# Optimization experiments

Measured on AMD Instinct MI355X. Metric: run time of the kernel, lower is better.

Reference implementation:

```python
import jax, jax.numpy as jnp
import numpy as np

HEAD_SIZE = 64

def setup_inputs() -> dict:
    key = jax.random.key(0)
    k1, k2, k3, k4 = jax.random.split(key, 4)
    B, S, D = 8, 2048, 1024
    scale = 1.0 / np.sqrt(D)
    x = jax.random.normal(k1, (B, S, D), dtype=jnp.float32)
    Wk = jax.random.normal(k2, (D, HEAD_SIZE), dtype=jnp.float32) * scale
    Wq = jax.random.normal(k3, (D, HEAD_SIZE), dtype=jnp.float32) * scale
    Wv = jax.random.normal(k4, (D, HEAD_SIZE), dtype=jnp.float32) * scale
    return {"x": x, "Wk": Wk, "Wq": Wq, "Wv": Wv}

def reference(x, Wk, Wq, Wv):
    # x: [B, S, D]; projections to [B, S, H]
    k = jnp.einsum('bsd,dh->bsh', x, Wk)
    q = jnp.einsum('bsd,dh->bsh', x, Wq)
    v = jnp.einsum('bsd,dh->bsh', x, Wv)
    H = q.shape[-1]
    scores = jnp.einsum('bqh,bkh->bqk', q, k) / jnp.sqrt(jnp.float32(H))  # [B,S,S]
    S = scores.shape[-1]
    causal = jnp.tril(jnp.ones((S, S), dtype=bool))
    scores = jnp.where(causal, scores, -jnp.inf)
    attn = jax.nn.softmax(scores, axis=-1)
    z = jnp.einsum('bqk,bkh->bqh', attn, v)  # [B,S,H]
    return z
```

## Files before the change

### kernel.cpp

```cpp
#include <hip/hip_runtime.h>
#include <hip/hip_bf16.h>

#define B_ 8
#define S_ 2048
#define D_ 1024
#define H_ 64

typedef __attribute__((ext_vector_type(8))) short bf16x8;
typedef __attribute__((ext_vector_type(4))) float f32x4;
typedef __attribute__((ext_vector_type(4))) unsigned short u16x4;
typedef unsigned short u16;
typedef unsigned int u32;

#define QSCALE 0.18033688011112042f

static __device__ __forceinline__ u16 f2bf(float f) {
  union { float f; unsigned u; } v; v.f = f;
  unsigned r = v.u + 0x7FFFu + ((v.u >> 16) & 1u);
  return (u16)(r >> 16);
}

__global__ __launch_bounds__(256) void wprep_kernel(const float* __restrict__ Wk,
                                                    const float* __restrict__ Wq,
                                                    const float* __restrict__ Wv,
                                                    u16* __restrict__ Wt) {
  __shared__ float lds[64][65];
  const int wsel = blockIdx.x >> 4;
  const int d0 = (blockIdx.x & 15) << 6;
  const float* W = (wsel == 0) ? Wq : ((wsel == 1) ? Wk : Wv);
  const int cbase = wsel << 6;
  const int tid = threadIdx.x;

#pragma unroll
  for (int e = 0; e < 16; ++e) {
    const int idx = e * 256 + tid;
    const int dd = idx >> 6, h = idx & 63;
    lds[dd][h] = W[(size_t)(d0 + dd) * H_ + h];
  }
  __syncthreads();
#pragma unroll
  for (int e = 0; e < 16; ++e) {
    const int idx = e * 256 + tid;
    const int c = idx >> 6, dd = idx & 63;
    Wt[(size_t)(cbase + c) * D_ + d0 + dd] = f2bf(lds[dd][c]);
  }
}

__global__ __launch_bounds__(512, 4) void qkv_kernel(const float* __restrict__ x,
                                                     const u16* __restrict__ Wt,
                                                     u16* __restrict__ Qb,
                                                     u16* __restrict__ Kb,
                                                     u16* __restrict__ Vt) {
  __shared__ char sh[65536];
  char* const xsb = sh;
  char* const wsb = sh + 16384;

  const int tid = threadIdx.x;
  const int w = tid >> 6;
  const int lane = tid & 63;
  const int r = lane & 15;
  const int g = lane >> 4;
  const int rg = w >> 2;
  const int cg = w & 3;

  const int bpin = blockIdx.x & 7;
  const int jj = blockIdx.x >> 3;
  const long row0 = ((long)bpin * 64 + jj) * 32;

#define STAGE_X(kc, buf)                                                       \
  {                                                                            \
    const char* gb = (const char*)x + (size_t)row0 * 4096 + (size_t)(kc) * 256;\
    const int L = tid * 16;                                                    \
    const int row = L >> 8;                                                    \
    const int sw = (L & 255) ^ ((row & 7) << 4);                               \
    __builtin_amdgcn_global_load_lds(                                          \
        (const __attribute__((address_space(1))) u32*)(gb + (size_t)row * 4096 + sw), \
        (__attribute__((address_space(3))) u32*)(xsb + (buf) * 8192 + L),      \
        16, 0, 0);                                                             \
  }

#define STAGE_W(kc, buf)                                                       \
  {                                                                            \
    const char* gb = (const char*)Wt + (size_t)(kc) * 128;                     \
    _Pragma("unroll") for (int j2 = 0; j2 < 3; ++j2) {                         \
      const int L = j2 * 8192 + tid * 16;                                      \
      const int col = L >> 7;                                                  \
      const int sw = (L & 127) ^ ((col & 7) << 4);                             \
      __builtin_amdgcn_global_load_lds(                                        \
          (const __attribute__((address_space(1))) u32*)(gb + (size_t)col * 2048 + sw), \
          (__attribute__((address_space(3))) u32*)(wsb + (buf) * 24576 + L),   \
          16, 0, 0);                                                           \
    }                                                                          \
  }

  f32x4 acc[3];
#pragma unroll
  for (int nf = 0; nf < 3; ++nf) acc[nf] = (f32x4){0.f, 0.f, 0.f, 0.f};

  STAGE_X(0, 0);
  STAGE_W(0, 0);
  int cur = 0;

  const int rr = rg * 16 + r;
  const int xswz = (rr & 7) << 4;

  for (int kc = 0; kc < 16; ++kc) {
    __syncthreads();
    if (kc < 15) {
      STAGE_X(kc + 1, cur ^ 1);
      STAGE_W(kc + 1, cur ^ 1);
    }
    __builtin_amdgcn_sched_barrier(0);

    const char* xb = xsb + cur * 8192;
    const char* wb = wsb + cur * 24576;
#pragma unroll
    for (int ks = 0; ks < 2; ++ks) {
      const int cb = ks * 128 + g * 32;
      const float4 lo = *(const float4*)(xb + rr * 256 + (cb ^ xswz));
      const float4 hi = *(const float4*)(xb + rr * 256 + ((cb + 16) ^ xswz));
      bf16x8 a;
      a[0] = (short)f2bf(lo.x); a[1] = (short)f2bf(lo.y);
      a[2] = (short)f2bf(lo.z); a[3] = (short)f2bf(lo.w);
      a[4] = (short)f2bf(hi.x); a[5] = (short)f2bf(hi.y);
      a[6] = (short)f2bf(hi.z); a[7] = (short)f2bf(hi.w);
#pragma unroll
      for (int nf = 0; nf < 3; ++nf) {
        const int col = cg * 48 + nf * 16 + r;
        const int wcb = (ks * 64 + g * 16) ^ ((col & 7) << 4);
        const bf16x8 b = *(const bf16x8*)(wb + col * 128 + wcb);
        acc[nf] = __builtin_amdgcn_mfma_f32_16x16x32_bf16(a, b, acc[nf], 0, 0, 0);
      }
    }
    cur ^= 1;
  }
#undef STAGE_W
#undef STAGE_X

  const int bb = (int)(row0 >> 11);
  const int srow = (int)(row0 & 2047) + rg * 16;
#pragma unroll
  for (int nf = 0; nf < 3; ++nf) {
    const int col = cg * 48 + nf * 16 + r;
    if (col < 64) {
#pragma unroll
      for (int ii = 0; ii < 4; ++ii)
        Qb[(row0 + rg * 16 + 4 * g + ii) * H_ + col] = f2bf(acc[nf][ii] * QSCALE);
    } else if (col < 128) {
#pragma unroll
      for (int ii = 0; ii < 4; ++ii)
        Kb[(row0 + rg * 16 + 4 * g + ii) * H_ + (col - 64)] = f2bf(acc[nf][ii]);
    } else {
      u16x4 vp;
#pragma unroll
      for (int ii = 0; ii < 4; ++ii) vp[ii] = f2bf(acc[nf][ii]);
      *(u16x4*)(Vt + ((size_t)(bb * H_ + (col - 128))) * S_ + srow + 4 * g) = vp;
    }
  }
}

__global__ __launch_bounds__(256, 2) void attn7_kernel(const u16* __restrict__ Qb,
                                                       const u16* __restrict__ Kb,
                                                       const u16* __restrict__ Vt,
                                                       float* __restrict__ out) {
  __shared__ u16 plds[4][16 * 72];
  __shared__ float plo[4][16][68];
  __shared__ float pml[4][2][16];

  const int b = blockIdx.x & 7;
  const int j = blockIdx.x >> 3;
  const int w = threadIdx.x >> 6;
  const int lane = threadIdx.x & 63;
  const int r = lane & 15;
  const int g = lane >> 4;

  const int qt = (w < 2) ? j : (127 - j);
  const int s = w & 1;
  const int q0 = qt << 4;
  const int T = (qt >> 2) + 1;
  const int half = (T + 1) >> 1;
  const int start = s ? half : 0;
  const int end = s ? T : half;

  const u16* Qp = Qb + ((long)(b * S_ + q0 + r)) * H_ + 8 * g;
  const bf16x8 bq0 = *(const bf16x8*)Qp;
  const bf16x8 bq1 = *(const bf16x8*)(Qp + 32);

  const u16* Kbase = Kb + (long)b * S_ * H_ + (long)r * H_ + 8 * g;
  const u16* Vbase = Vt + (long)b * H_ * S_ + (long)r * S_ + 8 * g;

  f32x4 o[4];
#pragma unroll
  for (int nf = 0; nf < 4; ++nf) o[nf] = (f32x4){0.f, 0.f, 0.f, 0.f};
  float m = -INFINITY, l = 0.f;

  u16* pw = plds[w];

  bf16x8 ka[8];
  if (start < end) {
    const int k0 = start << 6;
#pragma unroll
    for (int kf = 0; kf < 4; ++kf) {
      const u16* Kp = Kbase + (long)(k0 + kf * 16) * H_;
      ka[2 * kf] = *(const bf16x8*)(Kp);
      ka[2 * kf + 1] = *(const bf16x8*)(Kp + 32);
    }
  }

  for (int kt = start; kt < end; ++kt) {
    const int k0 = kt << 6;

    f32x4 t4[4];
    __builtin_amdgcn_s_setprio(1);
#pragma unroll
    for (int kf = 0; kf < 4; ++kf) {
      f32x4 t = (f32x4){0.f, 0.f, 0.f, 0.f};
      t = __builtin_amdgcn_mfma_f32_16x16x32_bf16(ka[2 * kf], bq0, t, 0, 0, 0);
      t = __builtin_amdgcn_mfma_f32_16x16x32_bf16(ka[2 * kf + 1], bq1, t, 0, 0, 0);
      t4[kf] = t;
    }
    __builtin_amdgcn_s_setprio(0);

    bf16x8 vv[8];
#pragma unroll
    for (int nf = 0; nf < 4; ++nf) {
      const u16* Vp = Vbase + (long)(nf * 16) * S_ + k0;
      vv[2 * nf] = *(const bf16x8*)(Vp);
      vv[2 * nf + 1] = *(const bf16x8*)(Vp + 32);
    }
    if (kt + 1 < end) {
      const int kn = (kt + 1) << 6;
#pragma unroll
      for (int kf = 0; kf < 4; ++kf) {
        const u16* Kp = Kbase + (long)(kn + kf * 16) * H_;
        ka[2 * kf] = *(const bf16x8*)(Kp);
        ka[2 * kf + 1] = *(const bf16x8*)(Kp + 32);
      }
    }

    if (kt == T - 1) {
#pragma unroll
      for (int kf = 0; kf < 4; ++kf)
#pragma unroll
        for (int i = 0; i < 4; ++i) {
          const int k = k0 + kf * 16 + 4 * g + i;
          if (k > q0 + r) t4[kf][i] = -INFINITY;
        }
    }

    float pm = t4[0][0];
#pragma unroll
    for (int kf = 0; kf < 4; ++kf)
#pragma unroll
      for (int i = 0; i < 4; ++i) pm = fmaxf(pm, t4[kf][i]);
    pm = fmaxf(pm, __shfl_xor(pm, 16));
    pm = fmaxf(pm, __shfl_xor(pm, 32));

    if (__any(pm > m + 8.f)) {
      const float mn = fmaxf(m, pm);
      const float sc = exp2f(m - mn);
      m = mn;
      l *= sc;
      float scr[4];
#pragma unroll
      for (int i = 0; i < 4; ++i) scr[i] = __shfl(sc, 4 * g + i);
#pragma unroll
      for (int nf = 0; nf < 4; ++nf)
#pragma unroll
        for (int i = 0; i < 4; ++i) o[nf][i] *= scr[i];
    }

    float ps = 0.f;
#pragma unroll
    for (int kf = 0; kf < 4; ++kf)
#pragma unroll
      for (int i = 0; i < 4; ++i) {
        const float p = exp2f(t4[kf][i] - m);
        t4[kf][i] = p;
        ps += p;
      }
    ps += __shfl_xor(ps, 16);
    ps += __shfl_xor(ps, 32);
    l += ps;

#pragma unroll
    for (int kf = 0; kf < 4; ++kf) {
      u16x4 pk;
#pragma unroll
      for (int i = 0; i < 4; ++i) pk[i] = f2bf(t4[kf][i]);
      *(u16x4*)(pw + r * 72 + kf * 16 + 4 * g) = pk;
    }

    const bf16x8 pa0 = *(const bf16x8*)(pw + r * 72 + 8 * g);
    const bf16x8 pa1 = *(const bf16x8*)(pw + r * 72 + 32 + 8 * g);

    __builtin_amdgcn_s_setprio(1);
#pragma unroll
    for (int nf = 0; nf < 4; ++nf) {
      o[nf] = __builtin_amdgcn_mfma_f32_16x16x32_bf16(pa0, vv[2 * nf], o[nf], 0, 0, 0);
      o[nf] = __builtin_amdgcn_mfma_f32_16x16x32_bf16(pa1, vv[2 * nf + 1], o[nf], 0, 0, 0);
    }
    __builtin_amdgcn_s_setprio(0);
  }

#pragma unroll
  for (int nf = 0; nf < 4; ++nf)
#pragma unroll
    for (int i = 0; i < 4; ++i)
      plo[w][4 * g + i][nf * 16 + r] = o[nf][i];
  if (g == 0) {
    pml[w][0][r] = m;
    pml[w][1][r] = l;
  }
  __syncthreads();

  const int base = (w >> 1) << 1;
  const int hlf = w & 1;
  const int qq0 = ((base == 0) ? j : (127 - j)) << 4;
#pragma unroll
  for (int rr = 0; rr < 8; ++rr) {
    const int row = hlf * 8 + rr;
    const float mA = pml[base][0][row], mB = pml[base + 1][0][row];
    const float lA = pml[base][1][row], lB = pml[base + 1][1][row];
    const float M = fmaxf(mA, mB);
    const float ea = exp2f(mA - M), eb = exp2f(mB - M);
    const float inv = 1.f / (lA * ea + lB * eb);
    const float oo = plo[base][row][lane] * ea + plo[base + 1][row][lane] * eb;
    out[((long)(b * S_ + qq0 + row)) * H_ + lane] = oo * inv;
  }
}

extern "C" void kernel_launch(void* const* d_in, const int* in_sizes, int n_in,
                              void* d_out, int out_size, void* d_ws, size_t ws_size,
                              hipStream_t stream) {
  const float* x  = (const float*)d_in[0];
  const float* Wk = (const float*)d_in[1];
  const float* Wq = (const float*)d_in[2];
  const float* Wv = (const float*)d_in[3];
  float* out = (float*)d_out;

  u16* Qb = (u16*)d_ws;
  u16* Kb = Qb + (long)B_ * S_ * H_;
  u16* Vt = Kb + (long)B_ * S_ * H_;
  u16* Wt = Vt + (long)B_ * S_ * H_;

  wprep_kernel<<<48, 256, 0, stream>>>(Wk, Wq, Wv, Wt);
  qkv_kernel<<<512, 512, 0, stream>>>(x, Wt, Qb, Kb, Vt);
  attn7_kernel<<<B_ * 64, 256, 0, stream>>>(Qb, Kb, Vt, out);
}
```

Measured before the change: 60.42 us.

## Pre-swizzle weights into MFMA fragment layout and load directly to registers in QKV projection

Measured after the change: 67.75 us. +12.1%, slower.

```diff
diff --git a/kernel.cpp b/kernel.cpp
--- a/kernel.cpp
+++ b/kernel.cpp
@@ -23,7 +23,7 @@
 __global__ __launch_bounds__(256) void wprep_kernel(const float* __restrict__ Wk,
                                                     const float* __restrict__ Wq,
                                                     const float* __restrict__ Wv,
-                                                    u16* __restrict__ Wt) {
+                                                    u16* __restrict__ Wt2) {
   __shared__ float lds[64][65];
   const int wsel = blockIdx.x >> 4;
   const int d0 = (blockIdx.x & 15) << 6;
@@ -34,122 +34,129 @@
 #pragma unroll
   for (int e = 0; e < 16; ++e) {
     const int idx = e * 256 + tid;
-    const int dd = idx >> 6, h = idx & 63;
-    lds[dd][h] = W[(size_t)(d0 + dd) * H_ + h];
+    lds[idx >> 6][idx & 63] = W[(size_t)(d0 + (idx >> 6)) * H_ + (idx & 63)];
   }
   __syncthreads();
-#pragma unroll
-  for (int e = 0; e < 16; ++e) {
-    const int idx = e * 256 + tid;
-    const int c = idx >> 6, dd = idx & 63;
-    Wt[(size_t)(cbase + c) * D_ + d0 + dd] = f2bf(lds[dd][c]);
-  }
-}
-
-__global__ __launch_bounds__(512, 4) void qkv_kernel(const float* __restrict__ x,
-                                                     const u16* __restrict__ Wt,
+
+#pragma unroll
+  for (int t2 = 0; t2 < 2; ++t2) {
+    const int idx = t2 * 256 + tid;
+    const int c_local = idx >> 3;
+    const int o = idx & 7;
+    const int c = cbase + c_local;
+    const int wv = c / 48, rem = c % 48;
+    const int nf = rem >> 4, rr = rem & 15;
+    const int k0 = d0 + o * 8;
+    const int step = k0 >> 5;
+    const int gg = (k0 >> 3) & 3;
+    u16 vals[8];
+#pragma unroll
+    for (int j = 0; j < 8; ++j) vals[j] = f2bf(lds[o * 8 + j][c_local]);
+    u16* dst = Wt2 + ((size_t)((step * 4 + wv) * 3 + nf) * 64 + gg * 16 + rr) * 8;
+    u16x4 v0 = {vals[0], vals[1], vals[2], vals[3]};
+    u16x4 v1 = {vals[4], vals[5], vals[6], vals[7]};
+    *(u16x4*)dst = v0;
+    *(u16x4*)(dst + 4) = v1;
+  }
+}
+
+__global__ __launch_bounds__(256, 2) void qkv_kernel(const float* __restrict__ x,
+                                                     const u16* __restrict__ Wt2,
                                                      u16* __restrict__ Qb,
                                                      u16* __restrict__ Kb,
                                                      u16* __restrict__ Vt) {
-  __shared__ char sh[65536];
-  char* const xsb = sh;
-  char* const wsb = sh + 16384;
+  __shared__ char xlds[65536];
 
   const int tid = threadIdx.x;
   const int w = tid >> 6;
   const int lane = tid & 63;
   const int r = lane & 15;
   const int g = lane >> 4;
-  const int rg = w >> 2;
-  const int cg = w & 3;
 
   const int bpin = blockIdx.x & 7;
   const int jj = blockIdx.x >> 3;
-  const long row0 = ((long)bpin * 64 + jj) * 32;
-
-#define STAGE_X(kc, buf)                                                       \
-  {                                                                            \
-    const char* gb = (const char*)x + (size_t)row0 * 4096 + (size_t)(kc) * 256;\
-    const int L = tid * 16;                                                    \
-    const int row = L >> 8;                                                    \
-    const int sw = (L & 255) ^ ((row & 7) << 4);                               \
-    __builtin_amdgcn_global_load_lds(                                          \
-        (const __attribute__((address_space(1))) u32*)(gb + (size_t)row * 4096 + sw), \
-        (__attribute__((address_space(3))) u32*)(xsb + (buf) * 8192 + L),      \
-        16, 0, 0);                                                             \
-  }
-
-#define STAGE_W(kc, buf)                                                       \
-  {                                                                            \
-    const char* gb = (const char*)Wt + (size_t)(kc) * 128;                     \
-    _Pragma("unroll") for (int j2 = 0; j2 < 3; ++j2) {                         \
-      const int L = j2 * 8192 + tid * 16;                                      \
-      const int col = L >> 7;                                                  \
-      const int sw = (L & 127) ^ ((col & 7) << 4);                             \
-      __builtin_amdgcn_global_load_lds(                                        \
-          (const __attribute__((address_space(1))) u32*)(gb + (size_t)col * 2048 + sw), \
-          (__attribute__((address_space(3))) u32*)(wsb + (buf) * 24576 + L),   \
-          16, 0, 0);                                                           \
-    }                                                                          \
+  const long row0 = ((long)bpin * 128 + jj) * 16;
+
+  {
+    const char* gb = (const char*)x + (size_t)row0 * 4096;
+#pragma unroll
+    for (int j = 0; j < 16; ++j) {
+      const int off = (tid * 16) ^ ((j & 7) << 4);
+      __builtin_amdgcn_global_load_lds(
+          (const __attribute__((address_space(1))) u32*)(gb + (size_t)j * 4096 + off),
+          (__attribute__((address_space(3))) u32*)(xlds + j * 4096 + tid * 16),
+          16, 0, 0);
+    }
   }
 
   f32x4 acc[3];
-#pragma unroll
-  for (int nf = 0; nf < 3; ++nf) acc[nf] = (f32x4){0.f, 0.f, 0.f, 0.f};
-
-  STAGE_X(0, 0);
-  STAGE_W(0, 0);
-  int cur = 0;
-
-  const int rr = rg * 16 + r;
-  const int xswz = (rr & 7) << 4;
-
-  for (int kc = 0; kc < 16; ++kc) {
-    __syncthreads();
-    if (kc < 15) {
-      STAGE_X(kc + 1, cur ^ 1);
-      STAGE_W(kc + 1, cur ^ 1);
-    }
-    __builtin_amdgcn_sched_barrier(0);
-
-    const char* xb = xsb + cur * 8192;
-    const char* wb = wsb + cur * 24576;
-#pragma unroll
-    for (int ks = 0; ks < 2; ++ks) {
-      const int cb = ks * 128 + g * 32;
-      const float4 lo = *(const float4*)(xb + rr * 256 + (cb ^ xswz));
-      const float4 hi = *(const float4*)(xb + rr * 256 + ((cb + 16) ^ xswz));
+  acc[0] = acc[1] = acc[2] = (f32x4){0.f, 0.f, 0.f, 0.f};
+
+  const u16* wp = Wt2 + (size_t)(w * 3) * 512 + lane * 8;
+  bf16x8 wA[3], wB[3];
+#pragma unroll
+  for (int nf = 0; nf < 3; ++nf) wA[nf] = *(const bf16x8*)(wp + nf * 512);
+#pragma unroll
+  for (int nf = 0; nf < 3; ++nf) wB[nf] = *(const bf16x8*)(wp + 6144 + nf * 512);
+
+  __syncthreads();
+
+  const int xswz = (r & 7) << 4;
+  const char* xrow = xlds + r * 4096;
+
+#pragma unroll
+  for (int s2 = 0; s2 < 16; ++s2) {
+    {
+      const int off = (2 * s2) * 128 + g * 32;
+      const float4 lo = *(const float4*)(xrow + (off ^ xswz));
+      const float4 hi = *(const float4*)(xrow + ((off + 16) ^ xswz));
       bf16x8 a;
       a[0] = (short)f2bf(lo.x); a[1] = (short)f2bf(lo.y);
       a[2] = (short)f2bf(lo.z); a[3] = (short)f2bf(lo.w);
       a[4] = (short)f2bf(hi.x); a[5] = (short)f2bf(hi.y);
       a[6] = (short)f2bf(hi.z); a[7] = (short)f2bf(hi.w);
 #pragma unroll
-      for (int nf = 0; nf < 3; ++nf) {
-        const int col = cg * 48 + nf * 16 + r;
-        const int wcb = (ks * 64 + g * 16) ^ ((col & 7) << 4);
-        const bf16x8 b = *(const bf16x8*)(wb + col * 128 + wcb);
-        acc[nf] = __builtin_amdgcn_mfma_f32_16x16x32_bf16(a, b, acc[nf], 0, 0, 0);
-      }
-    }
-    cur ^= 1;
-  }
-#undef STAGE_W
-#undef STAGE_X
-
-  const int bb = (int)(row0 >> 11);
-  const int srow = (int)(row0 & 2047) + rg * 16;
+      for (int nf = 0; nf < 3; ++nf)
+        acc[nf] = __builtin_amdgcn_mfma_f32_16x16x32_bf16(a, wA[nf], acc[nf], 0, 0, 0);
+    }
+    if (s2 < 15) {
+#pragma unroll
+      for (int nf = 0; nf < 3; ++nf)
+        wA[nf] = *(const bf16x8*)(wp + (size_t)(2 * s2 + 2) * 6144 + nf * 512);
+    }
+    {
+      const int off = (2 * s2 + 1) * 128 + g * 32;
+      const float4 lo = *(const float4*)(xrow + (off ^ xswz));
+      const float4 hi = *(const float4*)(xrow + ((off + 16) ^ xswz));
+      bf16x8 a;
+      a[0] = (short)f2bf(lo.x); a[1] = (short)f2bf(lo.y);
+      a[2] = (short)f2bf(lo.z); a[3] = (short)f2bf(lo.w);
+      a[4] = (short)f2bf(hi.x); a[5] = (short)f2bf(hi.y);
+      a[6] = (short)f2bf(hi.z); a[7] = (short)f2bf(hi.w);
+#pragma unroll
+      for (int nf = 0; nf < 3; ++nf)
+        acc[nf] = __builtin_amdgcn_mfma_f32_16x16x32_bf16(a, wB[nf], acc[nf], 0, 0, 0);
+    }
+    if (s2 < 15) {
+#pragma unroll
+      for (int nf = 0; nf < 3; ++nf)
+        wB[nf] = *(const bf16x8*)(wp + (size_t)(2 * s2 + 3) * 6144 + nf * 512);
+    }
+  }
+
+  const int bb = bpin;
+  const int srow = (int)(row0 & 2047);
 #pragma unroll
   for (int nf = 0; nf < 3; ++nf) {
-    const int col = cg * 48 + nf * 16 + r;
+    const int col = w * 48 + nf * 16 + r;
     if (col < 64) {
 #pragma unroll
       for (int ii = 0; ii < 4; ++ii)
-        Qb[(row0 + rg * 16 + 4 * g + ii) * H_ + col] = f2bf(acc[nf][ii] * QSCALE);
+        Qb[(row0 + 4 * g + ii) * H_ + col] = f2bf(acc[nf][ii] * QSCALE);
     } else if (col < 128) {
 #pragma unroll
       for (int ii = 0; ii < 4; ++ii)
-        Kb[(row0 + rg * 16 + 4 * g + ii) * H_ + (col - 64)] = f2bf(acc[nf][ii]);
+        Kb[(row0 + 4 * g + ii) * H_ + (col - 64)] = f2bf(acc[nf][ii]);
     } else {
       u16x4 vp;
 #pragma unroll
@@ -342,9 +349,9 @@
   u16* Qb = (u16*)d_ws;
   u16* Kb = Qb + (long)B_ * S_ * H_;
   u16* Vt = Kb + (long)B_ * S_ * H_;
-  u16* Wt = Vt + (long)B_ * S_ * H_;
-
-  wprep_kernel<<<48, 256, 0, stream>>>(Wk, Wq, Wv, Wt);
-  qkv_kernel<<<512, 512, 0, stream>>>(x, Wt, Qb, Kb, Vt);
+  u16* Wt2 = Vt + (long)B_ * S_ * H_;
+
+  wprep_kernel<<<48, 256, 0, stream>>>(Wk, Wq, Wv, Wt2);
+  qkv_kernel<<<1024, 256, 0, stream>>>(x, Wt2, Qb, Kb, Vt);
   attn7_kernel<<<B_ * 64, 256, 0, stream>>>(Qb, Kb, Vt, out);
 }
```

## Balance causal attention work evenly across four waves per block

Applied to the files above, without the earlier changes.

After: 61.03 us. About the same (+1.0%).

```diff
diff --git a/kernel.cpp b/kernel.cpp
--- a/kernel.cpp
+++ b/kernel.cpp
@@ -137,7 +137,7 @@
 #undef STAGE_W
 #undef STAGE_X
 
-  const int bb = (int)(row0 >> 11);
+  const int bb = bpin;
   const int srow = (int)(row0 & 2047) + rg * 16;
 #pragma unroll
   for (int nf = 0; nf < 3; ++nf) {
@@ -159,13 +159,13 @@
   }
 }
 
-__global__ __launch_bounds__(256, 2) void attn7_kernel(const u16* __restrict__ Qb,
+__global__ __launch_bounds__(256, 2) void attn9_kernel(const u16* __restrict__ Qb,
                                                        const u16* __restrict__ Kb,
                                                        const u16* __restrict__ Vt,
                                                        float* __restrict__ out) {
   __shared__ u16 plds[4][16 * 72];
-  __shared__ float plo[4][16][68];
-  __shared__ float pml[4][2][16];
+  __shared__ float plo[8][16][68];
+  __shared__ float pml[8][2][16];
 
   const int b = blockIdx.x & 7;
   const int j = blockIdx.x >> 3;
@@ -174,158 +174,165 @@
   const int r = lane & 15;
   const int g = lane >> 4;
 
-  const int qt = (w < 2) ? j : (127 - j);
-  const int s = w & 1;
-  const int q0 = qt << 4;
-  const int T = (qt >> 2) + 1;
-  const int half = (T + 1) >> 1;
-  const int start = s ? half : 0;
-  const int end = s ? T : half;
-
-  const u16* Qp = Qb + ((long)(b * S_ + q0 + r)) * H_ + 8 * g;
-  const bf16x8 bq0 = *(const bf16x8*)Qp;
-  const bf16x8 bq1 = *(const bf16x8*)(Qp + 32);
+  const int qtA = j, qtB = 127 - j;
+  const int T_A = (qtA >> 2) + 1;
+  const int T_B = (qtB >> 2) + 1;
+  const int start = (w * 33) >> 2;
+  const int end = ((w + 1) * 33) >> 2;
+
+  const u16* QpA = Qb + ((long)(b * S_ + (qtA << 4) + r)) * H_ + 8 * g;
+  const bf16x8 bqA0 = *(const bf16x8*)QpA;
+  const bf16x8 bqA1 = *(const bf16x8*)(QpA + 32);
+  const u16* QpB = Qb + ((long)(b * S_ + (qtB << 4) + r)) * H_ + 8 * g;
+  const bf16x8 bqB0 = *(const bf16x8*)QpB;
+  const bf16x8 bqB1 = *(const bf16x8*)(QpB + 32);
 
   const u16* Kbase = Kb + (long)b * S_ * H_ + (long)r * H_ + 8 * g;
   const u16* Vbase = Vt + (long)b * H_ * S_ + (long)r * S_ + 8 * g;
 
-  f32x4 o[4];
-#pragma unroll
-  for (int nf = 0; nf < 4; ++nf) o[nf] = (f32x4){0.f, 0.f, 0.f, 0.f};
-  float m = -INFINITY, l = 0.f;
-
   u16* pw = plds[w];
 
-  bf16x8 ka[8];
-  if (start < end) {
-    const int k0 = start << 6;
-#pragma unroll
-    for (int kf = 0; kf < 4; ++kf) {
-      const u16* Kp = Kbase + (long)(k0 + kf * 16) * H_;
-      ka[2 * kf] = *(const bf16x8*)(Kp);
-      ka[2 * kf + 1] = *(const bf16x8*)(Kp + 32);
-    }
-  }
-
-  for (int kt = start; kt < end; ++kt) {
-    const int k0 = kt << 6;
-
-    f32x4 t4[4];
-    __builtin_amdgcn_s_setprio(1);
-#pragma unroll
-    for (int kf = 0; kf < 4; ++kf) {
-      f32x4 t = (f32x4){0.f, 0.f, 0.f, 0.f};
-      t = __builtin_amdgcn_mfma_f32_16x16x32_bf16(ka[2 * kf], bq0, t, 0, 0, 0);
-      t = __builtin_amdgcn_mfma_f32_16x16x32_bf16(ka[2 * kf + 1], bq1, t, 0, 0, 0);
-      t4[kf] = t;
-    }
-    __builtin_amdgcn_s_setprio(0);
-
-    bf16x8 vv[8];
-#pragma unroll
-    for (int nf = 0; nf < 4; ++nf) {
-      const u16* Vp = Vbase + (long)(nf * 16) * S_ + k0;
-      vv[2 * nf] = *(const bf16x8*)(Vp);
-      vv[2 * nf + 1] = *(const bf16x8*)(Vp + 32);
-    }
-    if (kt + 1 < end) {
-      const int kn = (kt + 1) << 6;
-#pragma unroll
-      for (int kf = 0; kf < 4; ++kf) {
-        const u16* Kp = Kbase + (long)(kn + kf * 16) * H_;
-        ka[2 * kf] = *(const bf16x8*)(Kp);
-        ka[2 * kf + 1] = *(const bf16x8*)(Kp + 32);
-      }
-    }
-
-    if (kt == T - 1) {
-#pragma unroll
-      for (int kf = 0; kf < 4; ++kf)
-#pragma unroll
-        for (int i = 0; i < 4; ++i) {
-          const int k = k0 + kf * 16 + 4 * g + i;
-          if (k > q0 + r) t4[kf][i] = -INFINITY;
-        }
-    }
-
-    float pm = t4[0][0];
-#pragma unroll
-    for (int kf = 0; kf < 4; ++kf)
-#pragma unroll
-      for (int i = 0; i < 4; ++i) pm = fmaxf(pm, t4[kf][i]);
-    pm = fmaxf(pm, __shfl_xor(pm, 16));
-    pm = fmaxf(pm, __shfl_xor(pm, 32));
-
-    if (__any(pm > m + 8.f)) {
-      const float mn = fmaxf(m, pm);
-      const float sc = exp2f(m - mn);
-      m = mn;
-      l *= sc;
-      float scr[4];
-#pragma unroll
-      for (int i = 0; i < 4; ++i) scr[i] = __shfl(sc, 4 * g + i);
-#pragma unroll
-      for (int nf = 0; nf < 4; ++nf)
-#pragma unroll
-        for (int i = 0; i < 4; ++i) o[nf][i] *= scr[i];
-    }
-
-    float ps = 0.f;
-#pragma unroll
-    for (int kf = 0; kf < 4; ++kf)
-#pragma unroll
-      for (int i = 0; i < 4; ++i) {
-        const float p = exp2f(t4[kf][i] - m);
-        t4[kf][i] = p;
-        ps += p;
-      }
-    ps += __shfl_xor(ps, 16);
-    ps += __shfl_xor(ps, 32);
-    l += ps;
-
-#pragma unroll
-    for (int kf = 0; kf < 4; ++kf) {
-      u16x4 pk;
-#pragma unroll
-      for (int i = 0; i < 4; ++i) pk[i] = f2bf(t4[kf][i]);
-      *(u16x4*)(pw + r * 72 + kf * 16 + 4 * g) = pk;
-    }
-
-    const bf16x8 pa0 = *(const bf16x8*)(pw + r * 72 + 8 * g);
-    const bf16x8 pa1 = *(const bf16x8*)(pw + r * 72 + 32 + 8 * g);
-
-    __builtin_amdgcn_s_setprio(1);
-#pragma unroll
-    for (int nf = 0; nf < 4; ++nf) {
-      o[nf] = __builtin_amdgcn_mfma_f32_16x16x32_bf16(pa0, vv[2 * nf], o[nf], 0, 0, 0);
-      o[nf] = __builtin_amdgcn_mfma_f32_16x16x32_bf16(pa1, vv[2 * nf + 1], o[nf], 0, 0, 0);
-    }
-    __builtin_amdgcn_s_setprio(0);
-  }
-
-#pragma unroll
-  for (int nf = 0; nf < 4; ++nf)
-#pragma unroll
-    for (int i = 0; i < 4; ++i)
-      plo[w][4 * g + i][nf * 16 + r] = o[nf][i];
-  if (g == 0) {
-    pml[w][0][r] = m;
-    pml[w][1][r] = l;
-  }
+#define RANGE(q0, T, lo, hi, bq0, bq1)                                         \
+  if ((lo) < (hi)) {                                                           \
+    bf16x8 ka[8];                                                              \
+    {                                                                          \
+      const int k0 = (lo) << 6;                                                \
+      _Pragma("unroll") for (int kf = 0; kf < 4; ++kf) {                       \
+        const u16* Kp = Kbase + (long)(k0 + kf * 16) * H_;                     \
+        ka[2 * kf] = *(const bf16x8*)(Kp);                                     \
+        ka[2 * kf + 1] = *(const bf16x8*)(Kp + 32);                            \
+      }                                                                        \
+    }                                                                          \
+    for (int kt = (lo); kt < (hi); ++kt) {                                     \
+      const int k0 = kt << 6;                                                  \
+      f32x4 t4[4];                                                             \
+      __builtin_amdgcn_s_setprio(1);                                           \
+      _Pragma("unroll") for (int kf = 0; kf < 4; ++kf) {                       \
+        f32x4 t = (f32x4){0.f, 0.f, 0.f, 0.f};                                 \
+        t = __builtin_amdgcn_mfma_f32_16x16x32_bf16(ka[2 * kf], bq0, t, 0, 0, 0); \
+        t = __builtin_amdgcn_mfma_f32_16x16x32_bf16(ka[2 * kf + 1], bq1, t, 0, 0, 0); \
+        t4[kf] = t;                                                            \
+      }                                                                        \
+      __builtin_amdgcn_s_setprio(0);                                           \
+      bf16x8 vv[8];                                                            \
+      _Pragma("unroll") for (int nf = 0; nf < 4; ++nf) {                       \
+        const u16* Vp = Vbase + (long)(nf * 16) * S_ + k0;                     \
+        vv[2 * nf] = *(const bf16x8*)(Vp);                                     \
+        vv[2 * nf + 1] = *(const bf16x8*)(Vp + 32);                            \
+      }                                                                        \
+      if (kt + 1 < (hi)) {                                                     \
+        const int kn = (kt + 1) << 6;                                          \
+        _Pragma("unroll") for (int kf = 0; kf < 4; ++kf) {                     \
+          const u16* Kp = Kbase + (long)(kn + kf * 16) * H_;                   \
+          ka[2 * kf] = *(const bf16x8*)(Kp);                                   \
+          ka[2 * kf + 1] = *(const bf16x8*)(Kp + 32);                          \
+        }                                                                      \
+      }                                                                        \
+      if (kt == (T)-1) {                                                       \
+        _Pragma("unroll") for (int kf = 0; kf < 4; ++kf)                       \
+          _Pragma("unroll") for (int i = 0; i < 4; ++i) {                      \
+            const int k = k0 + kf * 16 + 4 * g + i;                            \
+            if (k > ((q0) << 4) + r) t4[kf][i] = -INFINITY;                    \
+          }                                                                    \
+      }                                                                        \
+      float pm = t4[0][0];                                                     \
+      _Pragma("unroll") for (int kf = 0; kf < 4; ++kf)                         \
+        _Pragma("unroll") for (int i = 0; i < 4; ++i) pm = fmaxf(pm, t4[kf][i]); \
+      pm = fmaxf(pm, __shfl_xor(pm, 16));                                      \
+      pm = fmaxf(pm, __shfl_xor(pm, 32));                                      \
+      if (__any(pm > m + 8.f)) {                                               \
+        const float mn = fmaxf(m, pm);                                         \
+        const float sc = exp2f(m - mn);                                        \
+        m = mn;                                                                \
+        l *= sc;                                                               \
+        float scr[4];                                                          \
+        _Pragma("unroll") for (int i = 0; i < 4; ++i) scr[i] = __shfl(sc, 4 * g + i); \
+        _Pragma("unroll") for (int nf = 0; nf < 4; ++nf)                       \
+          _Pragma("unroll") for (int i = 0; i < 4; ++i) o[nf][i] *= scr[i];    \
+      }                                                                        \
+      float ps = 0.f;                                                          \
+      _Pragma("unroll") for (int kf = 0; kf < 4; ++kf)                         \
+        _Pragma("unroll") for (int i = 0; i < 4; ++i) {                        \
+          const float p = exp2f(t4[kf][i] - m);                                \
+          t4[kf][i] = p;                                                       \
+          ps += p;                                                             \
+        }                                                                      \
+      ps += __shfl_xor(ps, 16);                                                \
+      ps += __shfl_xor(ps, 32);                                                \
+      l += ps;                                                                 \
+      _Pragma("unroll") for (int kf = 0; kf < 4; ++kf) {                       \
+        u16x4 pk;                                                              \
+        _Pragma("unroll") for (int i = 0; i < 4; ++i) pk[i] = f2bf(t4[kf][i]); \
+        *(u16x4*)(pw + r * 72 + kf * 16 + 4 * g) = pk;                         \
+      }                                                                        \
+      const bf16x8 pa0 = *(const bf16x8*)(pw + r * 72 + 8 * g);                \
+      const bf16x8 pa1 = *(const bf16x8*)(pw + r * 72 + 32 + 8 * g);           \
+      __builtin_amdgcn_s_setprio(1);                                           \
+      _Pragma("unroll") for (int nf = 0; nf < 4; ++nf) {                       \
+        o[nf] = __builtin_amdgcn_mfma_f32_16x16x32_bf16(pa0, vv[2 * nf], o[nf], 0, 0, 0); \
+        o[nf] = __builtin_amdgcn_mfma_f32_16x16x32_bf16(pa1, vv[2 * nf + 1], o[nf], 0, 0, 0); \
+      }                                                                        \
+      __builtin_amdgcn_s_setprio(0);                                           \
+    }                                                                          \
+  }
+
+  {
+    f32x4 o[4];
+#pragma unroll
+    for (int nf = 0; nf < 4; ++nf) o[nf] = (f32x4){0.f, 0.f, 0.f, 0.f};
+    float m = -INFINITY, l = 0.f;
+    const int loA = start;
+    const int hiA = (end < T_A) ? end : T_A;
+    RANGE(qtA, T_A, loA, hiA, bqA0, bqA1)
+#pragma unroll
+    for (int nf = 0; nf < 4; ++nf)
+#pragma unroll
+      for (int i = 0; i < 4; ++i)
+        plo[w][4 * g + i][nf * 16 + r] = o[nf][i];
+    if (g == 0) {
+      pml[w][0][r] = m;
+      pml[w][1][r] = l;
+    }
+  }
+
+  {
+    f32x4 o[4];
+#pragma unroll
+    for (int nf = 0; nf < 4; ++nf) o[nf] = (f32x4){0.f, 0.f, 0.f, 0.f};
+    float m = -INFINITY, l = 0.f;
+    const int loB = ((start > T_A) ? start : T_A) - T_A;
+    const int hiB = end - T_A;
+    RANGE(qtB, T_B, loB, hiB, bqB0, bqB1)
+#pragma unroll
+    for (int nf = 0; nf < 4; ++nf)
+#pragma unroll
+      for (int i = 0; i < 4; ++i)
+        plo[4 + w][4 * g + i][nf * 16 + r] = o[nf][i];
+    if (g == 0) {
+      pml[4 + w][0][r] = m;
+      pml[4 + w][1][r] = l;
+    }
+  }
+#undef RANGE
+
   __syncthreads();
 
-  const int base = (w >> 1) << 1;
-  const int hlf = w & 1;
-  const int qq0 = ((base == 0) ? j : (127 - j)) << 4;
-#pragma unroll
-  for (int rr = 0; rr < 8; ++rr) {
-    const int row = hlf * 8 + rr;
-    const float mA = pml[base][0][row], mB = pml[base + 1][0][row];
-    const float lA = pml[base][1][row], lB = pml[base + 1][1][row];
-    const float M = fmaxf(mA, mB);
-    const float ea = exp2f(mA - M), eb = exp2f(mB - M);
-    const float inv = 1.f / (lA * ea + lB * eb);
-    const float oo = plo[base][row][lane] * ea + plo[base + 1][row][lane] * eb;
+  const int sbase = (w >> 1) << 2;
+  const int qq0 = ((w >> 1) ? qtB : qtA) << 4;
+  const int rbase = (w & 1) * 8;
+#pragma unroll
+  for (int rr2 = 0; rr2 < 8; ++rr2) {
+    const int row = rbase + rr2;
+    const float m0 = pml[sbase][0][row], m1 = pml[sbase + 1][0][row];
+    const float m2 = pml[sbase + 2][0][row], m3 = pml[sbase + 3][0][row];
+    const float M = fmaxf(fmaxf(m0, m1), fmaxf(m2, m3));
+    const float e0 = exp2f(m0 - M), e1 = exp2f(m1 - M);
+    const float e2 = exp2f(m2 - M), e3 = exp2f(m3 - M);
+    const float L = pml[sbase][1][row] * e0 + pml[sbase + 1][1][row] * e1 +
+                    pml[sbase + 2][1][row] * e2 + pml[sbase + 3][1][row] * e3;
+    const float inv = 1.f / L;
+    const float oo = plo[sbase][row][lane] * e0 + plo[sbase + 1][row][lane] * e1 +
+                     plo[sbase + 2][row][lane] * e2 + plo[sbase + 3][row][lane] * e3;
     out[((long)(b * S_ + qq0 + row)) * H_ + lane] = oo * inv;
   }
 }
@@ -346,5 +353,5 @@
 
   wprep_kernel<<<48, 256, 0, stream>>>(Wk, Wq, Wv, Wt);
   qkv_kernel<<<512, 512, 0, stream>>>(x, Wt, Qb, Kb, Vt);
-  attn7_kernel<<<B_ * 64, 256, 0, stream>>>(Qb, Kb, Vt, out);
-}
+  attn9_kernel<<<B_ * 64, 256, 0, stream>>>(Qb, Kb, Vt, out);
+}
```
